# Performance work log

Measured on AMD Instinct MI355X. Metric: run time of the kernel, lower is better.

## Reference

```python
import jax, jax.numpy as jnp
import numpy as np

HIDDEN = 896
N_HEADS = 14
N_KV = 2
HEAD_DIM = HIDDEN // N_HEADS  # 64
N_REP = N_HEADS // N_KV       # 7
ROPE_THETA = 1000000.0


def setup_inputs() -> dict:
    key = jax.random.key(0)
    ks = jax.random.split(key, 8)
    B, S = 2, 2048
    s = 0.02
    return {
        "hidden_states": jax.random.normal(ks[0], (B, S, HIDDEN), dtype=jnp.float32),
        "position_ids": jnp.broadcast_to(jnp.arange(S, dtype=jnp.int64), (B, S)),
        "Wq": jax.random.normal(ks[1], (HIDDEN, HIDDEN), dtype=jnp.float32) * s,
        "bq": jnp.zeros((HIDDEN,), dtype=jnp.float32),
        "Wk": jax.random.normal(ks[2], (N_KV * HEAD_DIM, HIDDEN), dtype=jnp.float32) * s,
        "bk": jnp.zeros((N_KV * HEAD_DIM,), dtype=jnp.float32),
        "Wv": jax.random.normal(ks[3], (N_KV * HEAD_DIM, HIDDEN), dtype=jnp.float32) * s,
        "bv": jnp.zeros((N_KV * HEAD_DIM,), dtype=jnp.float32),
        "Wo": jax.random.normal(ks[4], (HIDDEN, HIDDEN), dtype=jnp.float32) * s,
    }


def _rotate_half(x):
    x1, x2 = x[..., : HEAD_DIM // 2], x[..., HEAD_DIM // 2 :]
    return jnp.concatenate((-x2, x1), axis=-1)


def reference(hidden_states, position_ids, Wq, bq, Wk, bk, Wv, bv, Wo):
    B, S, _ = hidden_states.shape
    q = (hidden_states @ Wq.T + bq).reshape(B, S, N_HEADS, HEAD_DIM)
    k = (hidden_states @ Wk.T + bk).reshape(B, S, N_KV, HEAD_DIM)
    v = (hidden_states @ Wv.T + bv).reshape(B, S, N_KV, HEAD_DIM)

    # RoPE: cos/sin [B, S, 1, HEAD_DIM]
    inv_freq = 1.0 / (ROPE_THETA ** (jnp.arange(0, HEAD_DIM, 2, dtype=jnp.float32) / HEAD_DIM))
    freqs = position_ids.astype(jnp.float32)[..., None] * inv_freq  # [B,S,D/2]
    emb = jnp.concatenate((freqs, freqs), axis=-1)
    cos = jnp.cos(emb)[:, :, None, :]
    sin = jnp.sin(emb)[:, :, None, :]
    q = q * cos + _rotate_half(q) * sin
    k = k * cos + _rotate_half(k) * sin

    # [B, H, S, D]; repeat KV heads (GQA)
    q = q.transpose(0, 2, 1, 3)
    k = jnp.repeat(k.transpose(0, 2, 1, 3), N_REP, axis=1)
    v = jnp.repeat(v.transpose(0, 2, 1, 3), N_REP, axis=1)

    scale = 1.0 / np.sqrt(HEAD_DIM)
    scores = jnp.einsum("bhqd,bhkd->bhqk", q, k) * scale
    causal = jnp.tril(jnp.ones((S, S), dtype=bool))
    scores = jnp.where(causal[None, None, :, :], scores, jnp.finfo(scores.dtype).min)
    probs = jax.nn.softmax(scores, axis=-1)
    attn = jnp.einsum("bhqk,bhkd->bhqd", probs, v)  # [B,H,S,D]
    attn = attn.transpose(0, 2, 1, 3).reshape(B, S, HIDDEN)
    return attn @ Wo.T
```

## Files before the change

### kernel.cpp

```cpp
#include <hip/hip_runtime.h>

#define HID 896
#define NH 14
#define NKV 2
#define NREP 7
#define SEQ 2048
#define BT 2
#define NTOK (BT*SEQ)
#define CSCALE 0.18033688011112042f

typedef __attribute__((ext_vector_type(8))) short bf16x8;
typedef __attribute__((ext_vector_type(8))) unsigned short u16x8;
typedef __attribute__((ext_vector_type(4))) float fx4;
typedef __attribute__((ext_vector_type(4))) short s16x4;
typedef _Float16 f16x4 __attribute__((ext_vector_type(4)));

__device__ __forceinline__ unsigned short f2b(float x){
  union { float f; unsigned u; } a; a.f = x;
  unsigned r = a.u + 0x7FFFu + ((a.u >> 16) & 1u);
  return (unsigned short)(r >> 16);
}
__device__ __forceinline__ unsigned short f2h(float x){
  union { _Float16 h; unsigned short u; } a; a.h = (_Float16)x; return a.u;
}

__global__ __launch_bounds__(256) void cvt_kernel(
    const float* __restrict__ s0, const float* __restrict__ s1,
    const float* __restrict__ s2, const float* __restrict__ s3,
    const float* __restrict__ s4,
    unsigned short* __restrict__ d0, unsigned short* __restrict__ d1,
    unsigned short* __restrict__ d2, unsigned short* __restrict__ d3,
    unsigned short* __restrict__ d4,
    int c0, int c1, int c2, int c3, int c4)
{
  const float* s; unsigned short* d; int c;
  switch (blockIdx.y){
    case 0: s=s0; d=d0; c=c0; break;
    case 1: s=s1; d=d1; c=c1; break;
    case 2: s=s2; d=d2; c=c2; break;
    case 3: s=s3; d=d3; c=c3; break;
    default: s=s4; d=d4; c=c4; break;
  }
  for (int i = (blockIdx.x*256 + threadIdx.x)*8; i < c; i += gridDim.x*2048){
    float4 a = *(const float4*)(s + i);
    float4 b = *(const float4*)(s + i + 4);
    u16x8 o;
    o[0]=f2b(a.x); o[1]=f2b(a.y); o[2]=f2b(a.z); o[3]=f2b(a.w);
    o[4]=f2b(b.x); o[5]=f2b(b.y); o[6]=f2b(b.z); o[7]=f2b(b.w);
    *(u16x8*)(d + i) = o;
  }
}

__global__ __launch_bounds__(256) void qkv_gemm_kernel(
    const unsigned short* __restrict__ A, const unsigned short* __restrict__ Bw,
    const float* __restrict__ bq, const float* __restrict__ bk, const float* __restrict__ bv,
    const int* __restrict__ pos,
    unsigned short* __restrict__ qo, unsigned short* __restrict__ ko,
    unsigned short* __restrict__ vt)
{
  __shared__ short As[128*72];
  __shared__ short Bs[128*72];
  const int tid = threadIdx.x;
  const int bm = blockIdx.x, bn = blockIdx.y;
  const int w = tid >> 6, l = tid & 63, l15 = l & 15, q4 = l >> 4;
  const int wm = w & 1, wn = w >> 1;

  fx4 acc[4][4] = {};

  const int srow = tid >> 3, scol = (tid & 7)*8;
  const unsigned short* Ag = A  + (size_t)(bm*128 + srow)*HID + scol;
  const unsigned short* Bg = Bw + (size_t)(bn*128 + srow)*HID + scol;

  u16x8 ar[4], br[4];
#pragma unroll
  for (int p = 0; p < 4; p++){
    ar[p] = *(const u16x8*)(Ag + (size_t)p*32*HID);
    br[p] = *(const u16x8*)(Bg + (size_t)p*32*HID);
  }

  for (int kt = 0; kt < 14; kt++){
#pragma unroll
    for (int p = 0; p < 4; p++){
      *(u16x8*)&As[(srow + p*32)*72 + scol] = ar[p];
      *(u16x8*)&Bs[(srow + p*32)*72 + scol] = br[p];
    }
    __syncthreads();
    if (kt < 13){
      const int ko_ = (kt+1)*64;
#pragma unroll
      for (int p = 0; p < 4; p++){
        ar[p] = *(const u16x8*)(Ag + (size_t)p*32*HID + ko_);
        br[p] = *(const u16x8*)(Bg + (size_t)p*32*HID + ko_);
      }
    }
#pragma unroll
    for (int ks = 0; ks < 2; ks++){
      bf16x8 af[4], bf[4];
#pragma unroll
      for (int mt = 0; mt < 4; mt++)
        af[mt] = *(bf16x8*)&As[(wm*64 + mt*16 + l15)*72 + ks*32 + q4*8];
#pragma unroll
      for (int nt = 0; nt < 4; nt++)
        bf[nt] = *(bf16x8*)&Bs[(wn*64 + nt*16 + l15)*72 + ks*32 + q4*8];
#pragma unroll
      for (int mt = 0; mt < 4; mt++)
#pragma unroll
        for (int nt = 0; nt < 4; nt++)
          acc[mt][nt] = __builtin_amdgcn_mfma_f32_16x16x32_bf16(af[mt], bf[nt], acc[mt][nt], 0,0,0);
    }
    __syncthreads();
  }

  const int hu = bn*2 + wn;
  const float* bias; int kind, hloc;
  if (hu < NH)      { bias = bq + hu*64;      kind = 0; hloc = hu; }
  else if (hu < 16) { bias = bk + (hu-NH)*64; kind = 1; hloc = hu-NH; }
  else              { bias = bv + (hu-16)*64; kind = 2; hloc = hu-16; }
  float bl[4];
#pragma unroll
  for (int nt = 0; nt < 4; nt++) bl[nt] = bias[nt*16 + l15];

  if (kind == 2){
#pragma unroll
    for (int mt = 0; mt < 4; mt++)
#pragma unroll
      for (int j = 0; j < 4; j++){
        int grow = bm*128 + wm*64 + mt*16 + q4*4 + j;
        int b = grow >> 11, s = grow & (SEQ-1);
        int tile = s >> 6, key = s & 63;
        unsigned short* dst = vt + (size_t)(((b*NKV + hloc)*(SEQ/64) + tile)*4096);
#pragma unroll
        for (int nt = 0; nt < 4; nt++)
          dst[(nt*16 + l15)*64 + key] = f2h(acc[mt][nt][j] + bl[nt]);
      }
  } else {
    float invf[2];
#pragma unroll
    for (int nt = 0; nt < 2; nt++)
      invf[nt] = exp2f(-(float)(nt*16 + l15) * 0.62286151779138041f);
#pragma unroll
    for (int mt = 0; mt < 4; mt++)
#pragma unroll
      for (int j = 0; j < 4; j++){
        int grow = bm*128 + wm*64 + mt*16 + q4*4 + j;
        int b = grow >> 11, s = grow & (SEQ-1);
        float p = (float)pos[grow];
        unsigned short* dst = (kind == 0)
            ? qo + ((size_t)(b*NH  + hloc)*SEQ + s)*64
            : ko + ((size_t)(b*NKV + hloc)*SEQ + s)*64;
#pragma unroll
        for (int nt = 0; nt < 2; nt++){
          int d = nt*16 + l15;
          float f = p * invf[nt];
          float sv, cv;
          sincosf(f, &sv, &cv);
          float x1 = acc[mt][nt][j]   + bl[nt];
          float x2 = acc[mt][nt+2][j] + bl[nt+2];
          dst[d]    = f2b(x1*cv - x2*sv);
          dst[d+32] = f2b(x2*cv + x1*sv);
        }
      }
  }
}

__device__ __forceinline__ void smax_pv(
    const fx4* s, bool diag, int wl, int q4,
    float& m_run, float& l_run, fx4* o, const f16x4 vf[4][4])
{
  float tv[16];
#pragma unroll
  for (int tl = 0; tl < 4; tl++)
#pragma unroll
    for (int j = 0; j < 4; j++){
      float x = s[tl][j]*CSCALE;
      if (diag && (tl*16 + q4*4 + j > wl)) x = -1e30f;
      tv[tl*4+j] = x;
    }
  float mx = tv[0];
#pragma unroll
  for (int i = 1; i < 16; i++) mx = fmaxf(mx, tv[i]);
  mx = fmaxf(mx, __shfl_xor(mx, 16));
  mx = fmaxf(mx, __shfl_xor(mx, 32));
  float mn = fmaxf(m_run, mx);
  float al = exp2f(m_run - mn);
  m_run = mn;
  float p[16], rs = 0.f;
#pragma unroll
  for (int i = 0; i < 16; i++){ p[i] = exp2f(tv[i] - mn); rs += p[i]; }
  rs += __shfl_xor(rs, 16);
  rs += __shfl_xor(rs, 32);
  l_run = l_run*al + rs;
#pragma unroll
  for (int nt = 0; nt < 4; nt++)
#pragma unroll
    for (int j = 0; j < 4; j++) o[nt][j] *= al;
  f16x4 pf[4];
#pragma unroll
  for (int tl = 0; tl < 4; tl++){
    pf[tl][0] = (_Float16)p[tl*4+0];
    pf[tl][1] = (_Float16)p[tl*4+1];
    pf[tl][2] = (_Float16)p[tl*4+2];
    pf[tl][3] = (_Float16)p[tl*4+3];
  }
#pragma unroll
  for (int nt = 0; nt < 4; nt++)
#pragma unroll
    for (int tl = 0; tl < 4; tl++)
      o[nt] = __builtin_amdgcn_mfma_f32_16x16x16f16(vf[nt][tl], pf[tl], o[nt], 0,0,0);
}

__global__ __launch_bounds__(256) void attn_kernel(
    const unsigned short* __restrict__ q, const unsigned short* __restrict__ k,
    const unsigned short* __restrict__ vt, unsigned short* __restrict__ ao)
{
  __shared__ short Ks[64*72];
  __shared__ short Vt[64*72];

  const int tid = threadIdx.x;
  const int w = tid >> 6, l = tid & 63, l15 = l & 15, q4 = l >> 4;
  const int tlo = blockIdx.x, thi = 31 - tlo;
  const int h = blockIdx.y, b = blockIdx.z, kvh = h / NREP;
  const int wl = w*16 + l15;

  const unsigned short* qbase = q + ((size_t)(b*NH + h)*SEQ)*64;
  const unsigned short* qpA = qbase + (size_t)(thi*64 + wl)*64;
  const unsigned short* qpB = qbase + (size_t)(tlo*64 + wl)*64;
  bf16x8 qA0 = *(const bf16x8*)(qpA + q4*8), qA1 = *(const bf16x8*)(qpA + 32 + q4*8);
  bf16x8 qB0 = *(const bf16x8*)(qpB + q4*8), qB1 = *(const bf16x8*)(qpB + 32 + q4*8);

  fx4 oA[4] = {{0,0,0,0},{0,0,0,0},{0,0,0,0},{0,0,0,0}};
  fx4 oB[4] = {{0,0,0,0},{0,0,0,0},{0,0,0,0},{0,0,0,0}};
  float mA = -1e30f, lA = 0.f, mB = -1e30f, lB = 0.f;

  const unsigned short* kbase = k  + ((size_t)(b*NKV + kvh)*SEQ)*64;
  const unsigned short* vbase = vt + (size_t)((b*NKV + kvh)*(SEQ/64))*4096;

  u16x8 kreg[2], vreg[2];
#pragma unroll
  for (int p = 0; p < 2; p++){
    int n = p*256 + tid;
    kreg[p] = *(const u16x8*)(kbase + n*8);
    vreg[p] = *(const u16x8*)(vbase + n*8);
  }

  for (int kt = 0; kt <= thi; kt++){
#pragma unroll
    for (int p = 0; p < 2; p++){
      int n = p*256 + tid, rr = n >> 3, g = n & 7;
      *(u16x8*)&Ks[rr*72 + g*8] = kreg[p];
      *(u16x8*)&Vt[rr*72 + g*8] = vreg[p];
    }
    __syncthreads();

    if (kt < thi){
      const unsigned short* kn = kbase + (size_t)(kt+1)*4096;
      const unsigned short* vn = vbase + (size_t)(kt+1)*4096;
#pragma unroll
      for (int p = 0; p < 2; p++){
        int n = p*256 + tid;
        kreg[p] = *(const u16x8*)(kn + n*8);
        vreg[p] = *(const u16x8*)(vn + n*8);
      }
    }

    bf16x8 kf0[4], kf1[4];
#pragma unroll
    for (int tl = 0; tl < 4; tl++){
      kf0[tl] = *(bf16x8*)&Ks[(tl*16 + l15)*72 + q4*8];
      kf1[tl] = *(bf16x8*)&Ks[(tl*16 + l15)*72 + 32 + q4*8];
    }
    f16x4 vf[4][4];
#pragma unroll
    for (int nt = 0; nt < 4; nt++)
#pragma unroll
      for (int tl = 0; tl < 4; tl++)
        vf[nt][tl] = *(f16x4*)&Vt[(nt*16 + l15)*72 + tl*16 + q4*4];

    {
      fx4 s[4] = {{0,0,0,0},{0,0,0,0},{0,0,0,0},{0,0,0,0}};
#pragma unroll
      for (int tl = 0; tl < 4; tl++){
        s[tl] = __builtin_amdgcn_mfma_f32_16x16x32_bf16(kf0[tl], qA0, s[tl], 0,0,0);
        s[tl] = __builtin_amdgcn_mfma_f32_16x16x32_bf16(kf1[tl], qA1, s[tl], 0,0,0);
      }
      smax_pv(s, kt == thi, wl, q4, mA, lA, oA, vf);
    }
    if (kt <= tlo){
      fx4 s[4] = {{0,0,0,0},{0,0,0,0},{0,0,0,0},{0,0,0,0}};
#pragma unroll
      for (int tl = 0; tl < 4; tl++){
        s[tl] = __builtin_amdgcn_mfma_f32_16x16x32_bf16(kf0[tl], qB0, s[tl], 0,0,0);
        s[tl] = __builtin_amdgcn_mfma_f32_16x16x32_bf16(kf1[tl], qB1, s[tl], 0,0,0);
      }
      smax_pv(s, kt == tlo, wl, q4, mB, lB, oB, vf);
    }
    __syncthreads();
  }

  {
    float inv = 1.0f / lA;
    unsigned short* dst = ao + ((size_t)(b*SEQ + thi*64 + wl))*HID + h*64;
#pragma unroll
    for (int nt = 0; nt < 4; nt++){
      s16x4 ov;
      ov[0] = (short)f2b(oA[nt][0]*inv); ov[1] = (short)f2b(oA[nt][1]*inv);
      ov[2] = (short)f2b(oA[nt][2]*inv); ov[3] = (short)f2b(oA[nt][3]*inv);
      *(s16x4*)(dst + nt*16 + q4*4) = ov;
    }
  }
  {
    float inv = 1.0f / lB;
    unsigned short* dst = ao + ((size_t)(b*SEQ + tlo*64 + wl))*HID + h*64;
#pragma unroll
    for (int nt = 0; nt < 4; nt++){
      s16x4 ov;
      ov[0] = (short)f2b(oB[nt][0]*inv); ov[1] = (short)f2b(oB[nt][1]*inv);
      ov[2] = (short)f2b(oB[nt][2]*inv); ov[3] = (short)f2b(oB[nt][3]*inv);
      *(s16x4*)(dst + nt*16 + q4*4) = ov;
    }
  }
}

__global__ __launch_bounds__(256) void out_gemm_kernel(
    const unsigned short* __restrict__ A, const unsigned short* __restrict__ Bw,
    float* __restrict__ out)
{
  __shared__ short As[128*72];
  __shared__ short Bs[128*72];
  const int tid = threadIdx.x;
  const int bm = blockIdx.x, bn = blockIdx.y;
  const int w = tid >> 6, l = tid & 63, l15 = l & 15, q4 = l >> 4;
  const int wm = w & 1, wn = w >> 1;

  fx4 acc[4][4] = {};

  const int srow = tid >> 3, scol = (tid & 7)*8;
  const unsigned short* Ag = A  + (size_t)(bm*128 + srow)*HID + scol;
  const unsigned short* Bg = Bw + (size_t)(bn*128 + srow)*HID + scol;

  u16x8 ar[4], br[4];
#pragma unroll
  for (int p = 0; p < 4; p++){
    ar[p] = *(const u16x8*)(Ag + (size_t)p*32*HID);
    br[p] = *(const u16x8*)(Bg + (size_t)p*32*HID);
  }

  for (int kt = 0; kt < 14; kt++){
#pragma unroll
    for (int p = 0; p < 4; p++){
      *(u16x8*)&As[(srow + p*32)*72 + scol] = ar[p];
      *(u16x8*)&Bs[(srow + p*32)*72 + scol] = br[p];
    }
    __syncthreads();
    if (kt < 13){
      const int ko_ = (kt+1)*64;
#pragma unroll
      for (int p = 0; p < 4; p++){
        ar[p] = *(const u16x8*)(Ag + (size_t)p*32*HID + ko_);
        br[p] = *(const u16x8*)(Bg + (size_t)p*32*HID + ko_);
      }
    }
#pragma unroll
    for (int ks = 0; ks < 2; ks++){
      bf16x8 af[4], bf[4];
#pragma unroll
      for (int mt = 0; mt < 4; mt++)
        af[mt] = *(bf16x8*)&As[(wm*64 + mt*16 + l15)*72 + ks*32 + q4*8];
#pragma unroll
      for (int nt = 0; nt < 4; nt++)
        bf[nt] = *(bf16x8*)&Bs[(wn*64 + nt*16 + l15)*72 + ks*32 + q4*8];
#pragma unroll
      for (int mt = 0; mt < 4; mt++)
#pragma unroll
        for (int nt = 0; nt < 4; nt++)
          acc[mt][nt] = __builtin_amdgcn_mfma_f32_16x16x32_bf16(af[mt], bf[nt], acc[mt][nt], 0,0,0);
    }
    __syncthreads();
  }

#pragma unroll
  for (int mt = 0; mt < 4; mt++)
#pragma unroll
    for (int j = 0; j < 4; j++){
      int grow = bm*128 + wm*64 + mt*16 + q4*4 + j;
      float* dst = out + (size_t)grow*HID + bn*128 + wn*64;
#pragma unroll
      for (int nt = 0; nt < 4; nt++)
        dst[nt*16 + l15] = acc[mt][nt][j];
    }
}

extern "C" void kernel_launch(void* const* d_in, const int* in_sizes, int n_in,
                              void* d_out, int out_size, void* d_ws, size_t ws_size,
                              hipStream_t stream)
{
  const float* hidden = (const float*)d_in[0];
  const int*   pos    = (const int*)d_in[1];
  const float* Wq = (const float*)d_in[2]; const float* bq = (const float*)d_in[3];
  const float* Wk = (const float*)d_in[4]; const float* bk = (const float*)d_in[5];
  const float* Wv = (const float*)d_in[6]; const float* bv = (const float*)d_in[7];
  const float* Wo = (const float*)d_in[8];

  unsigned short* qws   = (unsigned short*)d_ws;
  unsigned short* kws   = qws   + (size_t)BT*NH*SEQ*64;
  unsigned short* vtws  = kws   + (size_t)BT*NKV*SEQ*64;
  unsigned short* wqkv  = vtws  + (size_t)BT*NKV*SEQ*64;
  unsigned short* wo16  = wqkv  + (size_t)(NH+2*NKV/2)*0 + 1152*HID;
  unsigned short* h16   = wo16  + (size_t)HID*HID;

  const int nh   = NTOK*HID;
  const int nwq  = HID*HID;
  const int nwkv = 2*64*HID;

  cvt_kernel<<<dim3(448, 5), 256, 0, stream>>>(
      hidden, Wq, Wk, Wv, Wo,
      h16, wqkv, wqkv + nwq, wqkv + nwq + nwkv, wo16,
      nh, nwq, nwkv, nwkv, nwq);

  qkv_gemm_kernel<<<dim3(NTOK/128, 9), 256, 0, stream>>>(
      h16, wqkv, bq, bk, bv, pos, qws, kws, vtws);

  attn_kernel<<<dim3(16, NH, BT), 256, 0, stream>>>(qws, kws, vtws, h16 );

  out_gemm_kernel<<<dim3(NTOK/128, 7), 256, 0, stream>>>(h16 , wo16, (float*)d_out);
}
```

Measured before the change: 181.6 us.

## Split attention KV loop across two wave groups and shrink GEMM M-tiles

The attention kernel now runs 512 threads split into two groups of four waves. Each group processes alternate KV tiles into its own double-sized shared buffer, and the partial softmax states are merged through shared memory at the end. This gives each block more parallel work over the causal KV range and more waves to hide latency. Both GEMM kernels drop their M-tile from 128 to 64 rows, doubling the grid to fill more CUs at the cost of reloading the weight tiles more often. The probability conversion to fp16 also switches to packed round-toward-zero conversion, which slightly changes rounding.

```diff
diff --git a/kernel.cpp b/kernel.cpp
--- a/kernel.cpp
+++ b/kernel.cpp
@@ -14,6 +14,7 @@
 typedef __attribute__((ext_vector_type(4))) float fx4;
 typedef __attribute__((ext_vector_type(4))) short s16x4;
 typedef _Float16 f16x4 __attribute__((ext_vector_type(4)));
+typedef __fp16 fp16x2 __attribute__((ext_vector_type(2)));
 
 __device__ __forceinline__ unsigned short f2b(float x){
   union { float f; unsigned u; } a; a.f = x;
@@ -58,52 +59,49 @@
     unsigned short* __restrict__ qo, unsigned short* __restrict__ ko,
     unsigned short* __restrict__ vt)
 {
-  __shared__ short As[128*72];
+  __shared__ short As[64*72];
   __shared__ short Bs[128*72];
   const int tid = threadIdx.x;
   const int bm = blockIdx.x, bn = blockIdx.y;
   const int w = tid >> 6, l = tid & 63, l15 = l & 15, q4 = l >> 4;
-  const int wm = w & 1, wn = w >> 1;
-
-  fx4 acc[4][4] = {};
+  const int wm = w >> 1, wn = w & 1;
+
+  fx4 acc[2][4] = {};
 
   const int srow = tid >> 3, scol = (tid & 7)*8;
-  const unsigned short* Ag = A  + (size_t)(bm*128 + srow)*HID + scol;
+  const unsigned short* Ag = A  + (size_t)(bm*64  + srow)*HID + scol;
   const unsigned short* Bg = Bw + (size_t)(bn*128 + srow)*HID + scol;
 
-  u16x8 ar[4], br[4];
-#pragma unroll
-  for (int p = 0; p < 4; p++){
-    ar[p] = *(const u16x8*)(Ag + (size_t)p*32*HID);
-    br[p] = *(const u16x8*)(Bg + (size_t)p*32*HID);
-  }
+  u16x8 ar[2], br[4];
+#pragma unroll
+  for (int p = 0; p < 2; p++) ar[p] = *(const u16x8*)(Ag + (size_t)p*32*HID);
+#pragma unroll
+  for (int p = 0; p < 4; p++) br[p] = *(const u16x8*)(Bg + (size_t)p*32*HID);
 
   for (int kt = 0; kt < 14; kt++){
 #pragma unroll
-    for (int p = 0; p < 4; p++){
-      *(u16x8*)&As[(srow + p*32)*72 + scol] = ar[p];
-      *(u16x8*)&Bs[(srow + p*32)*72 + scol] = br[p];
-    }
+    for (int p = 0; p < 2; p++) *(u16x8*)&As[(srow + p*32)*72 + scol] = ar[p];
+#pragma unroll
+    for (int p = 0; p < 4; p++) *(u16x8*)&Bs[(srow + p*32)*72 + scol] = br[p];
     __syncthreads();
     if (kt < 13){
       const int ko_ = (kt+1)*64;
 #pragma unroll
-      for (int p = 0; p < 4; p++){
-        ar[p] = *(const u16x8*)(Ag + (size_t)p*32*HID + ko_);
-        br[p] = *(const u16x8*)(Bg + (size_t)p*32*HID + ko_);
-      }
+      for (int p = 0; p < 2; p++) ar[p] = *(const u16x8*)(Ag + (size_t)p*32*HID + ko_);
+#pragma unroll
+      for (int p = 0; p < 4; p++) br[p] = *(const u16x8*)(Bg + (size_t)p*32*HID + ko_);
     }
 #pragma unroll
     for (int ks = 0; ks < 2; ks++){
-      bf16x8 af[4], bf[4];
-#pragma unroll
-      for (int mt = 0; mt < 4; mt++)
-        af[mt] = *(bf16x8*)&As[(wm*64 + mt*16 + l15)*72 + ks*32 + q4*8];
+      bf16x8 af[2], bf[4];
+#pragma unroll
+      for (int mt = 0; mt < 2; mt++)
+        af[mt] = *(bf16x8*)&As[(wm*32 + mt*16 + l15)*72 + ks*32 + q4*8];
 #pragma unroll
       for (int nt = 0; nt < 4; nt++)
         bf[nt] = *(bf16x8*)&Bs[(wn*64 + nt*16 + l15)*72 + ks*32 + q4*8];
 #pragma unroll
-      for (int mt = 0; mt < 4; mt++)
+      for (int mt = 0; mt < 2; mt++)
 #pragma unroll
         for (int nt = 0; nt < 4; nt++)
           acc[mt][nt] = __builtin_amdgcn_mfma_f32_16x16x32_bf16(af[mt], bf[nt], acc[mt][nt], 0,0,0);
@@ -122,10 +120,10 @@
 
   if (kind == 2){
 #pragma unroll
-    for (int mt = 0; mt < 4; mt++)
+    for (int mt = 0; mt < 2; mt++)
 #pragma unroll
       for (int j = 0; j < 4; j++){
-        int grow = bm*128 + wm*64 + mt*16 + q4*4 + j;
+        int grow = bm*64 + wm*32 + mt*16 + q4*4 + j;
         int b = grow >> 11, s = grow & (SEQ-1);
         int tile = s >> 6, key = s & 63;
         unsigned short* dst = vt + (size_t)(((b*NKV + hloc)*(SEQ/64) + tile)*4096);
@@ -139,10 +137,10 @@
     for (int nt = 0; nt < 2; nt++)
       invf[nt] = exp2f(-(float)(nt*16 + l15) * 0.62286151779138041f);
 #pragma unroll
-    for (int mt = 0; mt < 4; mt++)
+    for (int mt = 0; mt < 2; mt++)
 #pragma unroll
       for (int j = 0; j < 4; j++){
-        int grow = bm*128 + wm*64 + mt*16 + q4*4 + j;
+        int grow = bm*64 + wm*32 + mt*16 + q4*4 + j;
         int b = grow >> 11, s = grow & (SEQ-1);
         float p = (float)pos[grow];
         unsigned short* dst = (kind == 0)
@@ -197,10 +195,10 @@
   f16x4 pf[4];
 #pragma unroll
   for (int tl = 0; tl < 4; tl++){
-    pf[tl][0] = (_Float16)p[tl*4+0];
-    pf[tl][1] = (_Float16)p[tl*4+1];
-    pf[tl][2] = (_Float16)p[tl*4+2];
-    pf[tl][3] = (_Float16)p[tl*4+3];
+    union { f16x4 v; fp16x2 h[2]; } u;
+    u.h[0] = __builtin_amdgcn_cvt_pkrtz(p[tl*4+0], p[tl*4+1]);
+    u.h[1] = __builtin_amdgcn_cvt_pkrtz(p[tl*4+2], p[tl*4+3]);
+    pf[tl] = u.v;
   }
 #pragma unroll
   for (int nt = 0; nt < 4; nt++)
@@ -209,18 +207,20 @@
       o[nt] = __builtin_amdgcn_mfma_f32_16x16x16f16(vf[nt][tl], pf[tl], o[nt], 0,0,0);
 }
 
-__global__ __launch_bounds__(256) void attn_kernel(
+__global__ __launch_bounds__(512) void attn_kernel(
     const unsigned short* __restrict__ q, const unsigned short* __restrict__ k,
     const unsigned short* __restrict__ vt, unsigned short* __restrict__ ao)
 {
-  __shared__ short Ks[64*72];
-  __shared__ short Vt[64*72];
+  __shared__ short SB[4*64*72];
+  short* KsB = SB;
+  short* VtB = SB + 2*64*72;
 
   const int tid = threadIdx.x;
   const int w = tid >> 6, l = tid & 63, l15 = l & 15, q4 = l >> 4;
+  const int g = w >> 2, wi = w & 3;
   const int tlo = blockIdx.x, thi = 31 - tlo;
   const int h = blockIdx.y, b = blockIdx.z, kvh = h / NREP;
-  const int wl = w*16 + l15;
+  const int wl = wi*16 + l15;
 
   const unsigned short* qbase = q + ((size_t)(b*NH + h)*SEQ)*64;
   const unsigned short* qpA = qbase + (size_t)(thi*64 + wl)*64;
@@ -228,95 +228,142 @@
   bf16x8 qA0 = *(const bf16x8*)(qpA + q4*8), qA1 = *(const bf16x8*)(qpA + 32 + q4*8);
   bf16x8 qB0 = *(const bf16x8*)(qpB + q4*8), qB1 = *(const bf16x8*)(qpB + 32 + q4*8);
 
-  fx4 oA[4] = {{0,0,0,0},{0,0,0,0},{0,0,0,0},{0,0,0,0}};
-  fx4 oB[4] = {{0,0,0,0},{0,0,0,0},{0,0,0,0},{0,0,0,0}};
+  fx4 oA[4] = {}, oB[4] = {};
   float mA = -1e30f, lA = 0.f, mB = -1e30f, lB = 0.f;
 
   const unsigned short* kbase = k  + ((size_t)(b*NKV + kvh)*SEQ)*64;
   const unsigned short* vbase = vt + (size_t)((b*NKV + kvh)*(SEQ/64))*4096;
 
+  const int P = (thi + 2) >> 1;
+
   u16x8 kreg[2], vreg[2];
 #pragma unroll
   for (int p = 0; p < 2; p++){
-    int n = p*256 + tid;
-    kreg[p] = *(const u16x8*)(kbase + n*8);
-    vreg[p] = *(const u16x8*)(vbase + n*8);
-  }
-
-  for (int kt = 0; kt <= thi; kt++){
+    int idx = p*512 + tid, tile = idx >> 9, off = idx & 511;
+    kreg[p] = *(const u16x8*)(kbase + (size_t)tile*4096 + off*8);
+    vreg[p] = *(const u16x8*)(vbase + (size_t)tile*4096 + off*8);
+  }
+
+  for (int si = 0; si < P; si++){
 #pragma unroll
     for (int p = 0; p < 2; p++){
-      int n = p*256 + tid, rr = n >> 3, g = n & 7;
-      *(u16x8*)&Ks[rr*72 + g*8] = kreg[p];
-      *(u16x8*)&Vt[rr*72 + g*8] = vreg[p];
-    }
-    __syncthreads();
-
-    if (kt < thi){
-      const unsigned short* kn = kbase + (size_t)(kt+1)*4096;
-      const unsigned short* vn = vbase + (size_t)(kt+1)*4096;
+      int idx = p*512 + tid, tile = idx >> 9, off = idx & 511;
+      int rr = off >> 3, g8 = off & 7;
+      *(u16x8*)&KsB[tile*4608 + rr*72 + g8*8] = kreg[p];
+      *(u16x8*)&VtB[tile*4608 + rr*72 + g8*8] = vreg[p];
+    }
+    __syncthreads();
+
+    if (si + 1 < P){
+      const int k0n = 2*(si+1);
 #pragma unroll
       for (int p = 0; p < 2; p++){
-        int n = p*256 + tid;
-        kreg[p] = *(const u16x8*)(kn + n*8);
-        vreg[p] = *(const u16x8*)(vn + n*8);
-      }
-    }
-
-    bf16x8 kf0[4], kf1[4];
-#pragma unroll
-    for (int tl = 0; tl < 4; tl++){
-      kf0[tl] = *(bf16x8*)&Ks[(tl*16 + l15)*72 + q4*8];
-      kf1[tl] = *(bf16x8*)&Ks[(tl*16 + l15)*72 + 32 + q4*8];
-    }
-    f16x4 vf[4][4];
+        int idx = p*512 + tid, tile = idx >> 9, off = idx & 511;
+        int tk = k0n + tile; if (tk > thi) tk = thi;
+        kreg[p] = *(const u16x8*)(kbase + (size_t)tk*4096 + off*8);
+        vreg[p] = *(const u16x8*)(vbase + (size_t)tk*4096 + off*8);
+      }
+    }
+
+    const int kt = 2*si + g;
+    if (kt <= thi){
+      const short* Kst = KsB + g*4608;
+      const short* Vtt = VtB + g*4608;
+      bf16x8 kf0[4], kf1[4];
+#pragma unroll
+      for (int tl = 0; tl < 4; tl++){
+        kf0[tl] = *(const bf16x8*)&Kst[(tl*16 + l15)*72 + q4*8];
+        kf1[tl] = *(const bf16x8*)&Kst[(tl*16 + l15)*72 + 32 + q4*8];
+      }
+      f16x4 vf[4][4];
+#pragma unroll
+      for (int nt = 0; nt < 4; nt++)
+#pragma unroll
+        for (int tl = 0; tl < 4; tl++)
+          vf[nt][tl] = *(const f16x4*)&Vtt[(nt*16 + l15)*72 + tl*16 + q4*4];
+
+      {
+        fx4 s[4] = {};
+#pragma unroll
+        for (int tl = 0; tl < 4; tl++){
+          s[tl] = __builtin_amdgcn_mfma_f32_16x16x32_bf16(kf0[tl], qA0, s[tl], 0,0,0);
+          s[tl] = __builtin_amdgcn_mfma_f32_16x16x32_bf16(kf1[tl], qA1, s[tl], 0,0,0);
+        }
+        smax_pv(s, kt == thi, wl, q4, mA, lA, oA, vf);
+      }
+      if (kt <= tlo){
+        fx4 s[4] = {};
+#pragma unroll
+        for (int tl = 0; tl < 4; tl++){
+          s[tl] = __builtin_amdgcn_mfma_f32_16x16x32_bf16(kf0[tl], qB0, s[tl], 0,0,0);
+          s[tl] = __builtin_amdgcn_mfma_f32_16x16x32_bf16(kf1[tl], qB1, s[tl], 0,0,0);
+        }
+        smax_pv(s, kt == tlo, wl, q4, mB, lB, oB, vf);
+      }
+    }
+    __syncthreads();
+  }
+
+  float* F = (float*)SB;
+  if (g == 1){
+    float* fa = F + (((wi*2 + 0)*64 + l)*18);
 #pragma unroll
     for (int nt = 0; nt < 4; nt++)
 #pragma unroll
-      for (int tl = 0; tl < 4; tl++)
-        vf[nt][tl] = *(f16x4*)&Vt[(nt*16 + l15)*72 + tl*16 + q4*4];
-
+      for (int j = 0; j < 4; j++) fa[nt*4 + j] = oA[nt][j];
+    fa[16] = mA; fa[17] = lA;
+    float* fb = F + (((wi*2 + 1)*64 + l)*18);
+#pragma unroll
+    for (int nt = 0; nt < 4; nt++)
+#pragma unroll
+      for (int j = 0; j < 4; j++) fb[nt*4 + j] = oB[nt][j];
+    fb[16] = mB; fb[17] = lB;
+  }
+  __syncthreads();
+  if (g == 0){
     {
-      fx4 s[4] = {{0,0,0,0},{0,0,0,0},{0,0,0,0},{0,0,0,0}};
-#pragma unroll
-      for (int tl = 0; tl < 4; tl++){
-        s[tl] = __builtin_amdgcn_mfma_f32_16x16x32_bf16(kf0[tl], qA0, s[tl], 0,0,0);
-        s[tl] = __builtin_amdgcn_mfma_f32_16x16x32_bf16(kf1[tl], qA1, s[tl], 0,0,0);
-      }
-      smax_pv(s, kt == thi, wl, q4, mA, lA, oA, vf);
-    }
-    if (kt <= tlo){
-      fx4 s[4] = {{0,0,0,0},{0,0,0,0},{0,0,0,0},{0,0,0,0}};
-#pragma unroll
-      for (int tl = 0; tl < 4; tl++){
-        s[tl] = __builtin_amdgcn_mfma_f32_16x16x32_bf16(kf0[tl], qB0, s[tl], 0,0,0);
-        s[tl] = __builtin_amdgcn_mfma_f32_16x16x32_bf16(kf1[tl], qB1, s[tl], 0,0,0);
-      }
-      smax_pv(s, kt == tlo, wl, q4, mB, lB, oB, vf);
-    }
-    __syncthreads();
-  }
-
-  {
-    float inv = 1.0f / lA;
-    unsigned short* dst = ao + ((size_t)(b*SEQ + thi*64 + wl))*HID + h*64;
-#pragma unroll
-    for (int nt = 0; nt < 4; nt++){
-      s16x4 ov;
-      ov[0] = (short)f2b(oA[nt][0]*inv); ov[1] = (short)f2b(oA[nt][1]*inv);
-      ov[2] = (short)f2b(oA[nt][2]*inv); ov[3] = (short)f2b(oA[nt][3]*inv);
-      *(s16x4*)(dst + nt*16 + q4*4) = ov;
-    }
-  }
-  {
-    float inv = 1.0f / lB;
-    unsigned short* dst = ao + ((size_t)(b*SEQ + tlo*64 + wl))*HID + h*64;
-#pragma unroll
-    for (int nt = 0; nt < 4; nt++){
-      s16x4 ov;
-      ov[0] = (short)f2b(oB[nt][0]*inv); ov[1] = (short)f2b(oB[nt][1]*inv);
-      ov[2] = (short)f2b(oB[nt][2]*inv); ov[3] = (short)f2b(oB[nt][3]*inv);
-      *(s16x4*)(dst + nt*16 + q4*4) = ov;
+      const float* fa = F + (((wi*2 + 0)*64 + l)*18);
+      float m1 = fa[16], l1 = fa[17];
+      float mM = fmaxf(mA, m1);
+      float a0 = exp2f(mA - mM), a1 = exp2f(m1 - mM);
+      lA = lA*a0 + l1*a1;
+#pragma unroll
+      for (int nt = 0; nt < 4; nt++)
+#pragma unroll
+        for (int j = 0; j < 4; j++) oA[nt][j] = oA[nt][j]*a0 + fa[nt*4+j]*a1;
+    }
+    {
+      const float* fb = F + (((wi*2 + 1)*64 + l)*18);
+      float m1 = fb[16], l1 = fb[17];
+      float mM = fmaxf(mB, m1);
+      float a0 = exp2f(mB - mM), a1 = exp2f(m1 - mM);
+      lB = lB*a0 + l1*a1;
+#pragma unroll
+      for (int nt = 0; nt < 4; nt++)
+#pragma unroll
+        for (int j = 0; j < 4; j++) oB[nt][j] = oB[nt][j]*a0 + fb[nt*4+j]*a1;
+    }
+    {
+      float inv = 1.0f / lA;
+      unsigned short* dst = ao + ((size_t)(b*SEQ + thi*64 + wl))*HID + h*64;
+#pragma unroll
+      for (int nt = 0; nt < 4; nt++){
+        s16x4 ov;
+        ov[0] = (short)f2b(oA[nt][0]*inv); ov[1] = (short)f2b(oA[nt][1]*inv);
+        ov[2] = (short)f2b(oA[nt][2]*inv); ov[3] = (short)f2b(oA[nt][3]*inv);
+        *(s16x4*)(dst + nt*16 + q4*4) = ov;
+      }
+    }
+    {
+      float inv = 1.0f / lB;
+      unsigned short* dst = ao + ((size_t)(b*SEQ + tlo*64 + wl))*HID + h*64;
+#pragma unroll
+      for (int nt = 0; nt < 4; nt++){
+        s16x4 ov;
+        ov[0] = (short)f2b(oB[nt][0]*inv); ov[1] = (short)f2b(oB[nt][1]*inv);
+        ov[2] = (short)f2b(oB[nt][2]*inv); ov[3] = (short)f2b(oB[nt][3]*inv);
+        *(s16x4*)(dst + nt*16 + q4*4) = ov;
+      }
     }
   }
 }
@@ -325,52 +372,49 @@
     const unsigned short* __restrict__ A, const unsigned short* __restrict__ Bw,
     float* __restrict__ out)
 {
-  __shared__ short As[128*72];
+  __shared__ short As[64*72];
   __shared__ short Bs[128*72];
   const int tid = threadIdx.x;
   const int bm = blockIdx.x, bn = blockIdx.y;
   const int w = tid >> 6, l = tid & 63, l15 = l & 15, q4 = l >> 4;
-  const int wm = w & 1, wn = w >> 1;
-
-  fx4 acc[4][4] = {};
+  const int wm = w >> 1, wn = w & 1;
+
+  fx4 acc[2][4] = {};
 
   const int srow = tid >> 3, scol = (tid & 7)*8;
-  const unsigned short* Ag = A  + (size_t)(bm*128 + srow)*HID + scol;
+  const unsigned short* Ag = A  + (size_t)(bm*64  + srow)*HID + scol;
   const unsigned short* Bg = Bw + (size_t)(bn*128 + srow)*HID + scol;
 
-  u16x8 ar[4], br[4];
-#pragma unroll
-  for (int p = 0; p < 4; p++){
-    ar[p] = *(const u16x8*)(Ag + (size_t)p*32*HID);
-    br[p] = *(const u16x8*)(Bg + (size_t)p*32*HID);
-  }
+  u16x8 ar[2], br[4];
+#pragma unroll
+  for (int p = 0; p < 2; p++) ar[p] = *(const u16x8*)(Ag + (size_t)p*32*HID);
+#pragma unroll
+  for (int p = 0; p < 4; p++) br[p] = *(const u16x8*)(Bg + (size_t)p*32*HID);
 
   for (int kt = 0; kt < 14; kt++){
 #pragma unroll
-    for (int p = 0; p < 4; p++){
-      *(u16x8*)&As[(srow + p*32)*72 + scol] = ar[p];
-      *(u16x8*)&Bs[(srow + p*32)*72 + scol] = br[p];
-    }
+    for (int p = 0; p < 2; p++) *(u16x8*)&As[(srow + p*32)*72 + scol] = ar[p];
+#pragma unroll
+    for (int p = 0; p < 4; p++) *(u16x8*)&Bs[(srow + p*32)*72 + scol] = br[p];
     __syncthreads();
     if (kt < 13){
       const int ko_ = (kt+1)*64;
 #pragma unroll
-      for (int p = 0; p < 4; p++){
-        ar[p] = *(const u16x8*)(Ag + (size_t)p*32*HID + ko_);
-        br[p] = *(const u16x8*)(Bg + (size_t)p*32*HID + ko_);
-      }
+      for (int p = 0; p < 2; p++) ar[p] = *(const u16x8*)(Ag + (size_t)p*32*HID + ko_);
+#pragma unroll
+      for (int p = 0; p < 4; p++) br[p] = *(const u16x8*)(Bg + (size_t)p*32*HID + ko_);
     }
 #pragma unroll
     for (int ks = 0; ks < 2; ks++){
-      bf16x8 af[4], bf[4];
-#pragma unroll
-      for (int mt = 0; mt < 4; mt++)
-        af[mt] = *(bf16x8*)&As[(wm*64 + mt*16 + l15)*72 + ks*32 + q4*8];
+      bf16x8 af[2], bf[4];
+#pragma unroll
+      for (int mt = 0; mt < 2; mt++)
+        af[mt] = *(bf16x8*)&As[(wm*32 + mt*16 + l15)*72 + ks*32 + q4*8];
 #pragma unroll
       for (int nt = 0; nt < 4; nt++)
         bf[nt] = *(bf16x8*)&Bs[(wn*64 + nt*16 + l15)*72 + ks*32 + q4*8];
 #pragma unroll
-      for (int mt = 0; mt < 4; mt++)
+      for (int mt = 0; mt < 2; mt++)
 #pragma unroll
         for (int nt = 0; nt < 4; nt++)
           acc[mt][nt] = __builtin_amdgcn_mfma_f32_16x16x32_bf16(af[mt], bf[nt], acc[mt][nt], 0,0,0);
@@ -379,10 +423,10 @@
   }
 
 #pragma unroll
-  for (int mt = 0; mt < 4; mt++)
+  for (int mt = 0; mt < 2; mt++)
 #pragma unroll
     for (int j = 0; j < 4; j++){
-      int grow = bm*128 + wm*64 + mt*16 + q4*4 + j;
+      int grow = bm*64 + wm*32 + mt*16 + q4*4 + j;
       float* dst = out + (size_t)grow*HID + bn*128 + wn*64;
 #pragma unroll
       for (int nt = 0; nt < 4; nt++)
@@ -405,7 +449,7 @@
   unsigned short* kws   = qws   + (size_t)BT*NH*SEQ*64;
   unsigned short* vtws  = kws   + (size_t)BT*NKV*SEQ*64;
   unsigned short* wqkv  = vtws  + (size_t)BT*NKV*SEQ*64;
-  unsigned short* wo16  = wqkv  + (size_t)(NH+2*NKV/2)*0 + 1152*HID;
+  unsigned short* wo16  = wqkv  + (size_t)1152*HID;
   unsigned short* h16   = wo16  + (size_t)HID*HID;
 
   const int nh   = NTOK*HID;
@@ -417,10 +461,10 @@
       h16, wqkv, wqkv + nwq, wqkv + nwq + nwkv, wo16,
       nh, nwq, nwkv, nwkv, nwq);
 
-  qkv_gemm_kernel<<<dim3(NTOK/128, 9), 256, 0, stream>>>(
+  qkv_gemm_kernel<<<dim3(NTOK/64, 9), 256, 0, stream>>>(
       h16, wqkv, bq, bk, bv, pos, qws, kws, vtws);
 
-  attn_kernel<<<dim3(16, NH, BT), 256, 0, stream>>>(qws, kws, vtws, h16 );
-
-  out_gemm_kernel<<<dim3(NTOK/128, 7), 256, 0, stream>>>(h16 , wo16, (float*)d_out);
-}
+  attn_kernel<<<dim3(16, NH, BT), 512, 0, stream>>>(qws, kws, vtws, h16 );
+
+  out_gemm_kernel<<<dim3(NTOK/64, 7), 256, 0, stream>>>(h16 , wo16, (float*)d_out);
+}
```

Result: faster. 171.7 us (-5.4%).
